# Performance work log

Measured on AMD Instinct MI355X. Metric: run time of the kernel, lower is better.

## Reference

```python
import jax, jax.numpy as jnp
import numpy as np

KERNEL = 7  # neighborhood window (7x7)
NUM_HEADS = 4


def _window_idx(L, k):
    # NATTEN edge-clamped window start: each query attends to exactly k neighbors.
    starts = jnp.clip(jnp.arange(L) - k // 2, 0, L - k)  # [L]
    return starts[:, None] + jnp.arange(k)[None, :]       # [L, k]


def setup_inputs() -> dict:
    key = jax.random.key(0)
    k1, k2, k3, k4, k5 = jax.random.split(key, 5)
    B, H, W, D = 8, 64, 64, 128
    return {
        "x": jax.random.normal(k1, (B, H, W, D), dtype=jnp.float32),
        "w_qkv": jax.random.normal(k2, (3 * D, D), dtype=jnp.float32) * 0.02,
        "b_qkv": jax.random.normal(k3, (3 * D,), dtype=jnp.float32) * 0.02,
        "w_proj": jax.random.normal(k4, (D, D), dtype=jnp.float32) * 0.02,
        "b_proj": jax.random.normal(k5, (D,), dtype=jnp.float32) * 0.02,
    }


def reference(x, w_qkv, b_qkv, w_proj, b_proj):
    B, H, W, D = x.shape
    nh, k = NUM_HEADS, KERNEL
    hd = D // nh
    scale = hd ** -0.5

    # QKV projection -> [3, B, nh, H, W, hd]
    qkv = x @ w_qkv.T + b_qkv
    qkv = qkv.reshape(B, H, W, 3, nh, hd).transpose(3, 0, 4, 1, 2, 5)
    q, kk, v = qkv[0], qkv[1], qkv[2]

    idx_h = _window_idx(H, k)  # [H, k]
    idx_w = _window_idx(W, k)  # [W, k]
    IH = idx_h[:, None, :, None]  # [H,1,k,1]
    IW = idx_w[None, :, None, :]  # [1,W,1,k]

    # Gather local K/V neighborhoods: [B, nh, H, W, k, k, hd] -> [B, nh, H, W, k*k, hd]
    kn = kk[:, :, IH, IW, :].reshape(B, nh, H, W, k * k, hd)
    vn = v[:, :, IH, IW, :].reshape(B, nh, H, W, k * k, hd)

    attn = jnp.einsum('bhxyd,bhxynd->bhxyn', q * scale, kn)
    attn = jax.nn.softmax(attn, axis=-1)
    out = jnp.einsum('bhxyn,bhxynd->bhxyd', attn, vn)

    out = out.transpose(0, 2, 3, 1, 4).reshape(B, H, W, D)
    return out @ w_proj.T + b_proj
```

## Files before the change

kernel.cpp:

```cpp
#include <hip/hip_runtime.h>
#include <hip/hip_bf16.h>

#define BB 8
#define HH 64
#define WW 64
#define DD 128
#define NH 4
#define HD 32
#define KS 7
#define TS 8
#define HALO 14

typedef __attribute__((ext_vector_type(8))) short short8v;
typedef __attribute__((ext_vector_type(4))) short short4v;
typedef __attribute__((ext_vector_type(4))) float f32x4;
typedef unsigned short bf16_t;

__device__ inline bf16_t f2bf(float f) {
  __hip_bfloat16 h = __float2bfloat16(f);
  return *reinterpret_cast<bf16_t*>(&h);
}

__global__ __launch_bounds__(256) void qkv_mfma(
    const float* __restrict__ x, const float* __restrict__ w,
    const float* __restrict__ bqkv,
    bf16_t* __restrict__ q, bf16_t* __restrict__ k, bf16_t* __restrict__ v) {
  __shared__ __align__(16) short smA[64 * 128];
  __shared__ __align__(16) short smB[128 * 128];
  const int tid = threadIdx.x;
  const int m_tile = blockIdx.x;
  const int n_tile = blockIdx.y;

  const float* Ab = x + (size_t)m_tile * 64 * 128;
  const float* Bb = w + (size_t)n_tile * 128 * 128;
#pragma unroll
  for (int i = 0; i < 4; i++) {
    int idx = tid + i * 256;
    int r = idx >> 4, p = idx & 15;
    const float* ap = Ab + r * 128 + p * 8;
    float4 a0 = *(const float4*)ap;
    float4 a1 = *(const float4*)(ap + 4);
    short8v s;
    s[0] = f2bf(a0.x); s[1] = f2bf(a0.y); s[2] = f2bf(a0.z); s[3] = f2bf(a0.w);
    s[4] = f2bf(a1.x); s[5] = f2bf(a1.y); s[6] = f2bf(a1.z); s[7] = f2bf(a1.w);
    *(short8v*)((char*)smA + ((r * 256 + p * 16) ^ ((r & 7) << 4))) = s;
  }
#pragma unroll
  for (int i = 0; i < 8; i++) {
    int idx = tid + i * 256;
    int r = idx >> 4, p = idx & 15;
    const float* bp_ = Bb + r * 128 + p * 8;
    float4 b0 = *(const float4*)bp_;
    float4 b1 = *(const float4*)(bp_ + 4);
    short8v t;
    t[0] = f2bf(b0.x); t[1] = f2bf(b0.y); t[2] = f2bf(b0.z); t[3] = f2bf(b0.w);
    t[4] = f2bf(b1.x); t[5] = f2bf(b1.y); t[6] = f2bf(b1.z); t[7] = f2bf(b1.w);
    *(short8v*)((char*)smB + ((r * 256 + p * 16) ^ ((r & 7) << 4))) = t;
  }
  __syncthreads();

  const int lane = tid & 63, wid = tid >> 6;
  const int wm = wid >> 1, wn = wid & 1;
  const int l15 = lane & 15, l4 = lane >> 4;

  f32x4 acc[2][4] = {};
  const int rowA0 = wm * 32 + l15;
  const int rowB0 = wn * 64 + l15;
  const int swzA = (rowA0 & 7) << 4;
  const int swzB = (rowB0 & 7) << 4;

#pragma unroll
  for (int ks = 0; ks < 4; ks++) {
    const int cb = ks * 64 + l4 * 16;
    short8v a[2], b[4];
#pragma unroll
    for (int mi = 0; mi < 2; mi++)
      a[mi] = *(const short8v*)((const char*)smA +
                ((((rowA0 + mi * 16) * 256) + cb) ^ swzA));
#pragma unroll
    for (int nj = 0; nj < 4; nj++)
      b[nj] = *(const short8v*)((const char*)smB +
                ((((rowB0 + nj * 16) * 256) + cb) ^ swzB));
#pragma unroll
    for (int mi = 0; mi < 2; mi++)
#pragma unroll
      for (int nj = 0; nj < 4; nj++)
        acc[mi][nj] = __builtin_amdgcn_mfma_f32_16x16x32_bf16(a[mi], b[nj], acc[mi][nj], 0, 0, 0);
  }

  __syncthreads();
  short* smC = smA;
  const float qscale = 0.17677669529663687f;
  const float sc = (n_tile == 0) ? qscale : 1.f;
#pragma unroll
  for (int nj = 0; nj < 4; nj++) {
    const int n_local = wn * 64 + nj * 16 + l15;
    const float bias = bqkv[n_tile * 128 + n_local];
#pragma unroll
    for (int mi = 0; mi < 2; mi++) {
#pragma unroll
      for (int r = 0; r < 4; r++) {
        const int m = wm * 32 + mi * 16 + l4 * 4 + r;
        *(bf16_t*)((char*)smC + ((m * 256 + n_local * 2) ^ ((m & 7) << 4))) =
            f2bf((acc[mi][nj][r] + bias) * sc);
      }
    }
  }
  __syncthreads();

  const int bblk = m_tile >> 6;
  bf16_t* outp = (n_tile == 0) ? q : ((n_tile == 1) ? k : v);
#pragma unroll
  for (int i = 0; i < 4; i++) {
    const int idx = i * 256 + tid;
    const int h = idx >> 8;
    const int rem = idx & 255;
    const int m = rem >> 2, c = rem & 3;
    short8v t8 = *(const short8v*)((const char*)smC +
        ((m * 256 + h * 64 + c * 16) ^ ((m & 7) << 4)));
    const int pix = (m_tile * 64 + m) & 4095;
    *(short8v*)(outp + ((size_t)(bblk * 4 + h)) * 131072 + (size_t)pix * 32 + c * 8) = t8;
  }
}

__global__ __launch_bounds__(256) void attn_proj_fused(
    const bf16_t* __restrict__ q, const bf16_t* __restrict__ k,
    const bf16_t* __restrict__ v, const float* __restrict__ wp,
    const float* __restrict__ bpj, float* __restrict__ out) {
  __shared__ __align__(16) char lds[49152];
  char* vtb = lds;
  short* wpb = (short*)(lds + 16384);

  const int tile = blockIdx.x;
  const int tx = tile >> 3, ty = tile & 7;
  const int bb = blockIdx.y;
  const int rstart = min(max(tx * TS - 3, 0), HH - HALO);
  const int cstart = min(max(ty * TS - 3, 0), WW - HALO);
  const int tid = threadIdx.x;
  const int lane = tid & 63, wid = tid >> 6;
  const int l15 = lane & 15, h4 = lane >> 4;
  const size_t bb4 = (size_t)bb * 4;

#pragma unroll
  for (int i = 0; i < 8; i++) {
    int idx = tid + i * 256;
    int r = idx >> 4, p = idx & 15;
    const float* bp_ = wp + r * 128 + p * 8;
    float4 b0 = *(const float4*)bp_;
    float4 b1 = *(const float4*)(bp_ + 4);
    short8v t;
    t[0] = f2bf(b0.x); t[1] = f2bf(b0.y); t[2] = f2bf(b0.z); t[3] = f2bf(b0.w);
    t[4] = f2bf(b1.x); t[5] = f2bf(b1.y); t[6] = f2bf(b1.z); t[7] = f2bf(b1.w);
    *(short8v*)((char*)wpb + ((r * 256 + p * 16) ^ ((r & 7) << 4))) = t;
  }

  int qx, qy;
  {
    const int pit = wid * 16 + l15;
    qx = tx * TS + (pit >> 3);
    qy = ty * TS + (pit & 7);
  }
  const size_t qoff = (size_t)(qx * WW + qy) * HD + h4 * 8;
  const int wx0 = min(max(qx - 3, 0), HH - KS) - rstart;
  const int wy0 = min(max(qy - 3, 0), WW - KS) - cstart;
  const int x0 = tx * TS + wid * 2;
  const int w0 = min(max(x0 - 3, 0), HH - KS) - rstart;
  const int base = min(w0 & ~1, 4);
  bool cv[4];
#pragma unroll
  for (int r = 0; r < 4; r++) cv[r] = ((unsigned)(h4 * 4 + r - wy0) < 7u);
  const int kcol = cstart + min(l15, 13);
  const f32x4 zf = {0.f, 0.f, 0.f, 0.f};

  short8v qf[4];
#pragma unroll
  for (int h = 0; h < 4; h++)
    qf[h] = *(const short8v*)(q + (bb4 + h) * 131072 + qoff);

  unsigned oph[4][4];

#pragma unroll
  for (int h = 0; h < 4; h++) {
    const bf16_t* kb = k + (bb4 + h) * 131072;
    const bf16_t* vb = v + (bb4 + h) * 131072;

    short4v vl[4][2];
#pragma unroll
    for (int t = 0; t < 4; t++) {
      const int idx = tid + t * 256;
      if (idx < 784) {
        const int pp = idx >> 3, c = idx & 7;
        const int pr = pp / 7, pc2 = (pp % 7) * 2;
        const size_t g = ((size_t)((rstart + pr) * WW + (cstart + pc2))) * HD + c * 4;
        vl[t][0] = *(const short4v*)(vb + g);
        vl[t][1] = *(const short4v*)(vb + g + HD);
      }
    }

    f32x4 acc[10];
#pragma unroll
    for (int ch = 0; ch < 2; ch++) {
      short8v kf[5];
#pragma unroll
      for (int i = 0; i < 5; i++) {
        const int pr = rstart + base + ch * 5 + i;
        kf[i] = *(const short8v*)(kb + ((size_t)(pr * WW + kcol)) * HD + h4 * 8);
      }
      __builtin_amdgcn_s_setprio(1);
#pragma unroll
      for (int i = 0; i < 5; i++)
        acc[ch * 5 + i] = __builtin_amdgcn_mfma_f32_16x16x32_bf16(kf[i], qf[h], zf, 0, 0, 0);
      __builtin_amdgcn_s_setprio(0);
    }

    if (h > 0) __syncthreads();

#pragma unroll
    for (int t = 0; t < 4; t++) {
      const int idx = tid + t * 256;
      if (idx < 784) {
        const int pp = idx >> 3, c = idx & 7;
        const int pr = pp / 7, pc2 = (pp % 7) * 2;
        const int pos0 = ((pr >> 1) << 5) + ((pc2 >> 2) << 3) + ((pr & 1) << 2) + (pc2 & 3);
#pragma unroll
        for (int j = 0; j < 4; j++) {
          const int d = c * 4 + j;
          const unsigned pk2 = (unsigned)(unsigned short)vl[t][0][j] |
                               ((unsigned)(unsigned short)vl[t][1][j] << 16);
          *(unsigned*)(vtb + ((d * 512 + pos0 * 2) ^ ((d & 7) << 4))) = pk2;
        }
      }
    }
    if (h == 0) {
      for (int idx = tid; idx < 512; idx += 256) {
        const int d = idx >> 4, pr = idx & 15;
        if (pr < 14) {
          const int pos = ((pr >> 1) << 5) + 24 + ((pr & 1) << 2) + 2;
          *(unsigned*)(vtb + ((d * 512 + pos * 2) ^ ((d & 7) << 4))) = 0u;
        }
      }
    }
    __syncthreads();

    float sum = 0.f;
#pragma unroll
    for (int nt = 0; nt < 10; nt++) {
      const bool rv = ((unsigned)(base + nt - wx0) < 7u);
#pragma unroll
      for (int r = 0; r < 4; r++) {
        const float p = (rv && cv[r]) ? __expf(acc[nt][r]) : 0.f;
        acc[nt][r] = p;
        sum += p;
      }
    }
    sum += __shfl_xor(sum, 16);
    sum += __shfl_xor(sum, 32);
    const float inv = 1.f / sum;

    f32x4 o0 = zf, o1 = zf;
    const int swzv = (l15 & 7) << 4;
    const int cbase = (base >> 1) * 64;
    __builtin_amdgcn_s_setprio(1);
#pragma unroll
    for (int kc = 0; kc < 5; kc++) {
      union { unsigned u[4]; short8v s; } pa;
      pa.u[0] = (unsigned)f2bf(acc[2 * kc][0] * inv) |
                ((unsigned)f2bf(acc[2 * kc][1] * inv) << 16);
      pa.u[1] = (unsigned)f2bf(acc[2 * kc][2] * inv) |
                ((unsigned)f2bf(acc[2 * kc][3] * inv) << 16);
      pa.u[2] = (unsigned)f2bf(acc[2 * kc + 1][0] * inv) |
                ((unsigned)f2bf(acc[2 * kc + 1][1] * inv) << 16);
      pa.u[3] = (unsigned)f2bf(acc[2 * kc + 1][2] * inv) |
                ((unsigned)f2bf(acc[2 * kc + 1][3] * inv) << 16);
      const int boff = cbase + kc * 64 + h4 * 16;
      short8v vb0 = *(const short8v*)(vtb + ((l15 * 512 + boff) ^ swzv));
      short8v vb1 = *(const short8v*)(vtb + (((l15 + 16) * 512 + boff) ^ swzv));
      o0 = __builtin_amdgcn_mfma_f32_16x16x32_bf16(pa.s, vb0, o0, 0, 0, 0);
      o1 = __builtin_amdgcn_mfma_f32_16x16x32_bf16(pa.s, vb1, o1, 0, 0, 0);
    }
    __builtin_amdgcn_s_setprio(0);

    oph[h][0] = (unsigned)f2bf(o0[0]) | ((unsigned)f2bf(o0[1]) << 16);
    oph[h][1] = (unsigned)f2bf(o0[2]) | ((unsigned)f2bf(o0[3]) << 16);
    oph[h][2] = (unsigned)f2bf(o1[0]) | ((unsigned)f2bf(o1[1]) << 16);
    oph[h][3] = (unsigned)f2bf(o1[2]) | ((unsigned)f2bf(o1[3]) << 16);
  }
  __syncthreads();

#pragma unroll
  for (int h = 0; h < 4; h++) {
#pragma unroll
    for (int j = 0; j < 4; j++) {
      const unsigned u = oph[h][j];
      const int row0 = wid * 16 + h4 * 4 + (j & 1) * 2;
      const int d = h * 32 + (j >> 1) * 16 + l15;
      *(bf16_t*)(vtb + ((row0 * 256 + d * 2) ^ ((row0 & 7) << 4))) = (bf16_t)(u & 0xFFFFu);
      const int row1 = row0 + 1;
      *(bf16_t*)(vtb + ((row1 * 256 + d * 2) ^ ((row1 & 7) << 4))) = (bf16_t)(u >> 16);
    }
  }
  __syncthreads();

  const int wm = wid >> 1, wn = wid & 1;
  const int l4 = lane >> 4;
  f32x4 pacc[2][4] = {};
  const int rowA0 = wm * 32 + l15;
  const int rowB0 = wn * 64 + l15;
  const int swzA = (rowA0 & 7) << 4;
  const int swzB = (rowB0 & 7) << 4;

#pragma unroll
  for (int ks = 0; ks < 4; ks++) {
    const int cb = ks * 64 + l4 * 16;
    short8v a[2], b[4];
#pragma unroll
    for (int mi = 0; mi < 2; mi++)
      a[mi] = *(const short8v*)(vtb + ((((rowA0 + mi * 16) * 256) + cb) ^ swzA));
#pragma unroll
    for (int nj = 0; nj < 4; nj++)
      b[nj] = *(const short8v*)((const char*)wpb +
                ((((rowB0 + nj * 16) * 256) + cb) ^ swzB));
    __builtin_amdgcn_s_setprio(1);
#pragma unroll
    for (int mi = 0; mi < 2; mi++)
#pragma unroll
      for (int nj = 0; nj < 4; nj++)
        pacc[mi][nj] = __builtin_amdgcn_mfma_f32_16x16x32_bf16(a[mi], b[nj], pacc[mi][nj], 0, 0, 0);
    __builtin_amdgcn_s_setprio(0);
  }

  __syncthreads();
  char* smC = lds + 16384;
#pragma unroll
  for (int nj = 0; nj < 4; nj++) {
    const int n = wn * 64 + nj * 16 + l15;
    const float bias = bpj[n];
#pragma unroll
    for (int mi = 0; mi < 2; mi++) {
#pragma unroll
      for (int r = 0; r < 4; r++) {
        const int m = wm * 32 + mi * 16 + l4 * 4 + r;
        *(float*)(smC + ((m * 512 + n * 4) ^ ((m & 7) << 5))) = pacc[mi][nj][r] + bias;
      }
    }
  }
  __syncthreads();

  float* obase = out + ((size_t)bb * 4096 + (size_t)(tx * TS) * WW + ty * TS) * DD;
#pragma unroll
  for (int i = 0; i < 8; i++) {
    const int idx = i * 256 + tid;
    const int m = idx >> 5, c = idx & 31;
    float4 t = *(const float4*)(smC + ((m * 512 + c * 16) ^ ((m & 7) << 5)));
    const size_t grow = (size_t)(m >> 3) * WW + (m & 7);
    *(float4*)(obase + grow * DD + c * 4) = t;
  }
}

extern "C" void kernel_launch(void* const* d_in, const int* in_sizes, int n_in,
                              void* d_out, int out_size, void* d_ws, size_t ws_size,
                              hipStream_t stream) {
  const float* x      = (const float*)d_in[0];
  const float* w_qkv  = (const float*)d_in[1];
  const float* b_qkv  = (const float*)d_in[2];
  const float* w_proj = (const float*)d_in[3];
  const float* b_proj = (const float*)d_in[4];
  float* out = (float*)d_out;

  const size_t per = (size_t)BB * NH * HH * WW * HD;
  bf16_t* q = (bf16_t*)d_ws;
  bf16_t* k = q + per;
  bf16_t* v = k + per;

  qkv_mfma<<<dim3(512, 3), dim3(256), 0, stream>>>(x, w_qkv, b_qkv, q, k, v);
  attn_proj_fused<<<dim3(64, BB), dim3(256), 0, stream>>>(q, k, v, w_proj, b_proj, out);
}
```

Before: 40.83 us.

## Prefetch next head's V tile into registers and use raw barriers

```diff
diff --git a/kernel.cpp b/kernel.cpp
--- a/kernel.cpp
+++ b/kernel.cpp
@@ -177,14 +177,9 @@
   for (int h = 0; h < 4; h++)
     qf[h] = *(const short8v*)(q + (bb4 + h) * 131072 + qoff);
 
-  unsigned oph[4][4];
-
-#pragma unroll
-  for (int h = 0; h < 4; h++) {
-    const bf16_t* kb = k + (bb4 + h) * 131072;
-    const bf16_t* vb = v + (bb4 + h) * 131072;
-
-    short4v vl[4][2];
+  short4v vlb[2][4][2];
+  {
+    const bf16_t* vb0 = v + bb4 * 131072;
 #pragma unroll
     for (int t = 0; t < 4; t++) {
       const int idx = tid + t * 256;
@@ -192,10 +187,17 @@
         const int pp = idx >> 3, c = idx & 7;
         const int pr = pp / 7, pc2 = (pp % 7) * 2;
         const size_t g = ((size_t)((rstart + pr) * WW + (cstart + pc2))) * HD + c * 4;
-        vl[t][0] = *(const short4v*)(vb + g);
-        vl[t][1] = *(const short4v*)(vb + g + HD);
-      }
-    }
+        vlb[0][t][0] = *(const short4v*)(vb0 + g);
+        vlb[0][t][1] = *(const short4v*)(vb0 + g + HD);
+      }
+    }
+  }
+
+  unsigned oph[4][4];
+
+#pragma unroll
+  for (int h = 0; h < 4; h++) {
+    const bf16_t* kb = k + (bb4 + h) * 131072;
 
     f32x4 acc[10];
 #pragma unroll
@@ -213,7 +215,11 @@
       __builtin_amdgcn_s_setprio(0);
     }
 
-    if (h > 0) __syncthreads();
+    if (h > 0) {
+      __builtin_amdgcn_sched_barrier(0);
+      __builtin_amdgcn_s_barrier();
+      __builtin_amdgcn_sched_barrier(0);
+    }
 
 #pragma unroll
     for (int t = 0; t < 4; t++) {
@@ -225,8 +231,8 @@
 #pragma unroll
         for (int j = 0; j < 4; j++) {
           const int d = c * 4 + j;
-          const unsigned pk2 = (unsigned)(unsigned short)vl[t][0][j] |
-                               ((unsigned)(unsigned short)vl[t][1][j] << 16);
+          const unsigned pk2 = (unsigned)(unsigned short)vlb[h & 1][t][0][j] |
+                               ((unsigned)(unsigned short)vlb[h & 1][t][1][j] << 16);
           *(unsigned*)(vtb + ((d * 512 + pos0 * 2) ^ ((d & 7) << 4))) = pk2;
         }
       }
@@ -240,7 +246,21 @@
         }
       }
     }
-    __syncthreads();
+
+    if (h < 3) {
+      const bf16_t* vbn = v + (bb4 + h + 1) * 131072;
+#pragma unroll
+      for (int t = 0; t < 4; t++) {
+        const int idx = tid + t * 256;
+        if (idx < 784) {
+          const int pp = idx >> 3, c = idx & 7;
+          const int pr = pp / 7, pc2 = (pp % 7) * 2;
+          const size_t g = ((size_t)((rstart + pr) * WW + (cstart + pc2))) * HD + c * 4;
+          vlb[(h + 1) & 1][t][0] = *(const short4v*)(vbn + g);
+          vlb[(h + 1) & 1][t][1] = *(const short4v*)(vbn + g + HD);
+        }
+      }
+    }
 
     float sum = 0.f;
 #pragma unroll
@@ -256,6 +276,11 @@
     sum += __shfl_xor(sum, 16);
     sum += __shfl_xor(sum, 32);
     const float inv = 1.f / sum;
+
+    asm volatile("s_waitcnt lgkmcnt(0)" ::: "memory");
+    __builtin_amdgcn_sched_barrier(0);
+    __builtin_amdgcn_s_barrier();
+    __builtin_amdgcn_sched_barrier(0);
 
     f32x4 o0 = zf, o1 = zf;
     const int swzv = (l15 & 7) << 4;
```

Result: no change. 40.48 us, median of 3 (-0.9%).
